# Performance work log

Measured on AMD Instinct MI355X. Metric: run time of the kernel, lower is better.

## Reference

```python
import jax, jax.numpy as jnp
import numpy as np

N_NODES, N_EDGES = 100000, 800000
F_NODE, F_EDGE, N_CLASSES = 128, 16, 10


def _lin(key, fan_in, fan_out, bias=True):
    k1, k2 = jax.random.split(key)
    W = jax.random.normal(k1, (fan_in, fan_out), jnp.float32) * 0.05
    if bias:
        b = jax.random.normal(k2, (fan_out,), jnp.float32) * 0.05
        return W, b
    return (W,)


def setup_inputs() -> dict:
    key = jax.random.key(0)
    ks = jax.random.split(key, 24)
    inp = {
        "x": jax.random.normal(ks[0], (N_NODES, F_NODE), jnp.float32),
        "edge_index": jax.random.randint(ks[1], (2, N_EDGES), 0, N_NODES, jnp.int64 if jax.config.jax_enable_x64 else jnp.int32),
        "edge_attr": jax.random.normal(ks[2], (N_EDGES, F_EDGE), jnp.float32),
    }
    dims = [(F_NODE, 128), (128, 128), (128, 256)]  # (in_channels, out_channels) per layer
    i = 3
    for li, (din, dout) in enumerate(dims, start=1):
        inp[f"Wq{li}"], inp[f"bq{li}"] = _lin(ks[i], din, dout); i += 1
        inp[f"Wk{li}"], inp[f"bk{li}"] = _lin(ks[i], din, dout); i += 1
        inp[f"Wv{li}"], inp[f"bv{li}"] = _lin(ks[i], din, dout); i += 1
        (inp[f"We{li}"],) = _lin(ks[i], F_EDGE, dout, bias=False); i += 1  # PyG lin_edge: bias=False
        inp[f"Ws{li}"], inp[f"bs{li}"] = _lin(ks[i], din, dout); i += 1  # root/skip weight
    inp["Wc"], inp["bc"] = _lin(ks[i], 256, N_CLASSES)
    return inp


def transformer_conv(x, src, dst, edge_attr, Wq, bq, Wk, bk, Wv, bv, We, Ws, bs):
    """PyG TransformerConv, heads=1, concat=True, root_weight=True."""
    N = x.shape[0]
    C = Wq.shape[1]
    q = x @ Wq + bq                      # [N, C]
    k = x @ Wk + bk                      # [N, C]
    v = x @ Wv + bv                      # [N, C]
    e = edge_attr @ We                   # [E, C] edge-conditioned term
    # per-edge attention logits: <q_i, k_j + e_ij> / sqrt(C)
    alpha = jnp.sum(q[dst] * (k[src] + e), axis=-1) / jnp.sqrt(jnp.float32(C))  # [E]
    # segment softmax over edges sharing a destination node
    m = jax.ops.segment_max(alpha, dst, num_segments=N)
    p = jnp.exp(alpha - m[dst])
    s = jax.ops.segment_sum(p, dst, num_segments=N)
    a = p / (s[dst] + 1e-16)
    # scatter-aggregate weighted messages (value_j + edge term)
    out = jax.ops.segment_sum(a[:, None] * (v[src] + e), dst, num_segments=N)  # [N, C]
    return out + x @ Ws + bs             # root/skip connection


def reference(x, edge_index, edge_attr,
              Wq1, bq1, Wk1, bk1, Wv1, bv1, We1, Ws1, bs1,
              Wq2, bq2, Wk2, bk2, Wv2, bv2, We2, Ws2, bs2,
              Wq3, bq3, Wk3, bk3, Wv3, bv3, We3, Ws3, bs3,
              Wc, bc):
    src, dst = edge_index[0], edge_index[1]
    h = transformer_conv(x, src, dst, edge_attr, Wq1, bq1, Wk1, bk1, Wv1, bv1, We1, Ws1, bs1)
    h = jax.nn.relu(h)  # dropout is identity in eval mode
    h = transformer_conv(h, src, dst, edge_attr, Wq2, bq2, Wk2, bk2, Wv2, bv2, We2, Ws2, bs2)
    h = jax.nn.relu(h)
    h = transformer_conv(h, src, dst, edge_attr, Wq3, bq3, Wk3, bk3, Wv3, bv3, We3, Ws3, bs3)
    return h @ Wc + bc                   # [N, num_classes]
```

## Files before the change

### kernel.cpp

```cpp
#include <hip/hip_runtime.h>
#include <math.h>


typedef unsigned int uint;
typedef unsigned short ushort;
typedef __bf16 bf16x8 __attribute__((ext_vector_type(8)));
typedef float f32x4 __attribute__((ext_vector_type(4)));

__device__ __forceinline__ ushort f2bf(float f) {
    uint u = __float_as_uint(f);
    u += 0x7fffu + ((u >> 16) & 1u);
    return (ushort)(u >> 16);
}
__device__ __forceinline__ float bf2f(ushort h) {
    return __uint_as_float(((uint)h) << 16);
}

__global__ void k_zero(uint* p, int n) {
    int i = blockIdx.x * 256 + threadIdx.x;
    if (i < n) p[i] = 0u;
}

__global__ void k_hist(const int* __restrict__ dst, uint* __restrict__ counts, int E, int N) {
    int e = blockIdx.x * 256 + threadIdx.x;
    if (e < E) {
        int d = dst[e];
        d = (d < 0) ? 0 : (d >= N ? N - 1 : d);
        atomicAdd(&counts[d], 1u);
    }
}

__global__ void k_scan1(const uint* __restrict__ counts, uint* __restrict__ bsum, int n) {
    __shared__ uint sm[256];
    int tid = threadIdx.x;
    int base = blockIdx.x * 1024 + tid * 4;
    uint s = 0;
#pragma unroll
    for (int j = 0; j < 4; ++j)
        if (base + j < n) s += counts[base + j];
    sm[tid] = s;
    __syncthreads();
    for (int d = 128; d > 0; d >>= 1) {
        if (tid < d) sm[tid] += sm[tid + d];
        __syncthreads();
    }
    if (tid == 0) bsum[blockIdx.x] = sm[0];
}

__global__ void k_scan2(uint* bsum, int nb) {
    if (threadIdx.x == 0 && blockIdx.x == 0) {
        uint run = 0;
        for (int i = 0; i < nb; ++i) { uint v = bsum[i]; bsum[i] = run; run += v; }
    }
}

__global__ void k_scan3(const uint* __restrict__ counts, const uint* __restrict__ bsum,
                        uint* __restrict__ row_ptr, int n, int E) {
    __shared__ uint sm[256];
    int tid = threadIdx.x;
    int base = blockIdx.x * 1024 + tid * 4;
    uint local[4];
    uint s = 0;
#pragma unroll
    for (int j = 0; j < 4; ++j) {
        local[j] = (base + j < n) ? counts[base + j] : 0u;
        s += local[j];
    }
    sm[tid] = s;
    __syncthreads();
    for (int d = 1; d < 256; d <<= 1) {
        uint v = (tid >= d) ? sm[tid - d] : 0u;
        __syncthreads();
        sm[tid] += v;
        __syncthreads();
    }
    uint run = sm[tid] - s + bsum[blockIdx.x];
#pragma unroll
    for (int j = 0; j < 4; ++j)
        if (base + j < n) { row_ptr[base + j] = run; run += local[j]; }
    if (blockIdx.x == 0 && tid == 0) row_ptr[n] = (uint)E;
}

__global__ void k_fill(const int* __restrict__ ei, const uint* __restrict__ row_ptr,
                       uint* __restrict__ cursor, int2* __restrict__ srcid, int E, int N) {
    int e = blockIdx.x * 256 + threadIdx.x;
    if (e >= E) return;
    int s = ei[e];
    int d = ei[E + e];
    s = (s < 0) ? 0 : (s >= N ? N - 1 : s);
    d = (d < 0) ? 0 : (d >= N ? N - 1 : d);
    uint idx = row_ptr[d] + atomicAdd(&cursor[d], 1u);
    srcid[idx] = make_int2(s, e);
}

__global__ void k_cvt(const float4* __restrict__ in, ushort4* __restrict__ outp, int n4) {
    int i = blockIdx.x * 256 + threadIdx.x;
    if (i >= n4) return;
    float4 v = in[i];
    ushort4 o;
    o.x = f2bf(v.x); o.y = f2bf(v.y); o.z = f2bf(v.z); o.w = f2bf(v.w);
    outp[i] = o;
}

__global__ void k_packg(const float* __restrict__ Wq, const float* __restrict__ bq,
                        const float* __restrict__ We, float* __restrict__ Wgf,
                        float* __restrict__ bgf, int C) {
    int id = blockIdx.x * 256 + threadIdx.x;
    if (id < 2048) {
        int k = id >> 4, f = id & 15;
        float s = 0.f;
        for (int c = 0; c < C; ++c) s = fmaf(Wq[k * C + c], We[f * C + c], s);
        Wgf[id] = s;
    } else if (id < 2064) {
        int f = id - 2048;
        float s = 0.f;
        for (int c = 0; c < C; ++c) s = fmaf(bq[c], We[f * C + c], s);
        bgf[f] = s;
    }
}

__global__ void k_packw(const float* __restrict__ Wq, const float* __restrict__ Wk,
                        const float* __restrict__ Wv, const float* __restrict__ Ws,
                        const float* __restrict__ Wgf, ushort* __restrict__ Bp, int C) {
    int nct = (4 * C + 16) >> 4;
    int total = 4 * nct * 512;
    int id = blockIdx.x * 256 + threadIdx.x;
    if (id >= total) return;
    int j = id & 7;
    int rest = id >> 3;
    int lane = rest & 63;
    rest >>= 6;
    int ct = rest % nct;
    int kt = rest / nct;
    int k = kt * 32 + ((lane >> 4) << 3) + j;
    int c = (ct << 4) + (lane & 15);
    float w;
    if (c < 4 * C) {
        int mat = c / C, cc = c % C;
        const float* W = (mat == 0) ? Wq : (mat == 1) ? Wk : (mat == 2) ? Wv : Ws;
        w = W[k * C + cc];
    } else {
        w = Wgf[k * 16 + (c - 4 * C)];
    }
    Bp[id] = f2bf(w);
}

__global__ void k_bias(const float* __restrict__ bq, const float* __restrict__ bk,
                       const float* __restrict__ bv, const float* __restrict__ bs,
                       const float* __restrict__ bgf, float* __restrict__ outp, int C) {
    int c = blockIdx.x * 256 + threadIdx.x;
    if (c >= 4 * C + 16) return;
    float v;
    if (c < 4 * C) {
        int mat = c / C, cc = c % C;
        const float* b = (mat == 0) ? bq : (mat == 1) ? bk : (mat == 2) ? bv : bs;
        v = b[cc];
    } else {
        v = bgf[c - 4 * C];
    }
    outp[c] = v;
}

__global__ __launch_bounds__(256) void k_gemm(const ushort* __restrict__ A,
                                              const ushort* __restrict__ Bp,
                                              const float* __restrict__ bias,
                                              ushort* __restrict__ H,
                                              ushort* __restrict__ S,
                                              ushort* __restrict__ g, int C) {
    int fourC = 4 * C, threeC = 3 * C;
    int P = fourC + 16;
    int nct = P >> 4;
    int lane = threadIdx.x & 63;
    int wave = threadIdx.x >> 6;
    int quad = lane >> 4;
    int r = lane & 15;
    int m0 = blockIdx.y << 4;
    int c0 = (blockIdx.x << 8) + (wave << 6);
    int ct0 = c0 >> 4;
    if (ct0 >= nct) return;
    int row = m0 + r;

    f32x4 acc[4];
#pragma unroll
    for (int i = 0; i < 4; ++i) acc[i] = (f32x4){0.f, 0.f, 0.f, 0.f};

#pragma unroll
    for (int kk = 0; kk < 4; ++kk) {
        bf16x8 a = *(const bf16x8*)(A + (size_t)row * 128 + kk * 32 + (quad << 3));
#pragma unroll
        for (int i = 0; i < 4; ++i) {
            if (ct0 + i < nct) {
                bf16x8 b = *(const bf16x8*)(Bp + ((size_t)((kk * nct + ct0 + i) << 6) + lane) * 8);
                acc[i] = __builtin_amdgcn_mfma_f32_16x16x32_bf16(a, b, acc[i], 0, 0, 0);
            }
        }
    }
#pragma unroll
    for (int i = 0; i < 4; ++i) {
        int cc = c0 + (i << 4) + r;
        if (cc >= P) continue;
        float bi = bias[cc];
#pragma unroll
        for (int reg = 0; reg < 4; ++reg) {
            int rr = m0 + (quad << 2) + reg;
            ushort val = f2bf(acc[i][reg] + bi);
            if (cc < threeC)      H[(size_t)rr * threeC + cc] = val;
            else if (cc < fourC)  S[(size_t)rr * C + (cc - threeC)] = val;
            else                  g[(size_t)rr * 16 + (cc - fourC)] = val;
        }
    }
}

template <int VPL>
__device__ __forceinline__ void loadbf(const ushort* p, float* o);
template <>
__device__ __forceinline__ void loadbf<2>(const ushort* p, float* o) {
    uint u = *(const uint*)p;
    o[0] = bf2f((ushort)(u & 0xffffu));
    o[1] = bf2f((ushort)(u >> 16));
}
template <>
__device__ __forceinline__ void loadbf<4>(const ushort* p, float* o) {
    uint2 u = *(const uint2*)p;
    o[0] = bf2f((ushort)(u.x & 0xffffu));
    o[1] = bf2f((ushort)(u.x >> 16));
    o[2] = bf2f((ushort)(u.y & 0xffffu));
    o[3] = bf2f((ushort)(u.y >> 16));
}

template <int C, bool RELU>
__global__ __launch_bounds__(256) void k_edge(const ushort* __restrict__ H,
                                              ushort* __restrict__ S,
                                              const ushort* __restrict__ g,
                                              const uint* __restrict__ row_ptr,
                                              const int2* __restrict__ srcid,
                                              const float* __restrict__ eattr,
                                              const float* __restrict__ We,
                                              int N, int totalWaves) {
    constexpr int VPL = C / 64;
    constexpr int THREEC = 3 * C;
    __shared__ float sWe[16 * C];
    for (int idx = threadIdx.x; idx < 16 * C; idx += 256) sWe[idx] = We[idx];
    __syncthreads();

    int lane = threadIdx.x & 63;
    int f16 = lane & 15;
    int gw = (int)((blockIdx.x * blockDim.x + threadIdx.x) >> 6);
    const float scale = (C == 128) ? 0.08838834764831843f : 0.0625f;

    for (int node = gw; node < N; node += totalWaves) {
        uint beg = row_ptr[node], end = row_ptr[node + 1];
        float q[VPL];
        loadbf<VPL>(H + (size_t)node * THREEC + lane * VPL, q);
        float gl = bf2f(g[(size_t)node * 16 + f16]);
        float m = -INFINITY, l = 0.f, w = 0.f;
        float acc[VPL];
#pragma unroll
        for (int j = 0; j < VPL; ++j) acc[j] = 0.f;

        for (uint t = beg; t < end; t += 4) {
            int rem = (int)(end - t);
            int2 se0 = srcid[t];
            int2 se1 = srcid[(rem > 1) ? t + 1 : t];
            int2 se2 = srcid[(rem > 2) ? t + 2 : t];
            int2 se3 = srcid[(rem > 3) ? t + 3 : t];
            float at0 = eattr[(size_t)se0.y * 16 + f16];
            float at1 = eattr[(size_t)se1.y * 16 + f16];
            float at2 = eattr[(size_t)se2.y * 16 + f16];
            float at3 = eattr[(size_t)se3.y * 16 + f16];
            float kv0[VPL], kv1[VPL], kv2[VPL], kv3[VPL];
            float vv0[VPL], vv1[VPL], vv2[VPL], vv3[VPL];
            loadbf<VPL>(H + (size_t)se0.x * THREEC + C + lane * VPL, kv0);
            loadbf<VPL>(H + (size_t)se1.x * THREEC + C + lane * VPL, kv1);
            loadbf<VPL>(H + (size_t)se2.x * THREEC + C + lane * VPL, kv2);
            loadbf<VPL>(H + (size_t)se3.x * THREEC + C + lane * VPL, kv3);
            loadbf<VPL>(H + (size_t)se0.x * THREEC + 2 * C + lane * VPL, vv0);
            loadbf<VPL>(H + (size_t)se1.x * THREEC + 2 * C + lane * VPL, vv1);
            loadbf<VPL>(H + (size_t)se2.x * THREEC + 2 * C + lane * VPL, vv2);
            loadbf<VPL>(H + (size_t)se3.x * THREEC + 2 * C + lane * VPL, vv3);
            float p0 = 0.25f * at0 * gl;
            float p1 = 0.25f * at1 * gl;
            float p2 = 0.25f * at2 * gl;
            float p3 = 0.25f * at3 * gl;
#pragma unroll
            for (int j = 0; j < VPL; ++j) {
                p0 = fmaf(q[j], kv0[j], p0);
                p1 = fmaf(q[j], kv1[j], p1);
                p2 = fmaf(q[j], kv2[j], p2);
                p3 = fmaf(q[j], kv3[j], p3);
            }
#pragma unroll
            for (int off = 32; off > 0; off >>= 1) {
                p0 += __shfl_xor(p0, off);
                p1 += __shfl_xor(p1, off);
                p2 += __shfl_xor(p2, off);
                p3 += __shfl_xor(p3, off);
            }
            float a0 = p0 * scale;
            float a1 = (rem > 1) ? p1 * scale : -INFINITY;
            float a2 = (rem > 2) ? p2 * scale : -INFINITY;
            float a3 = (rem > 3) ? p3 * scale : -INFINITY;
            float mn = fmaxf(m, fmaxf(fmaxf(a0, a1), fmaxf(a2, a3)));
            float sc = __expf(m - mn);
            float e0 = __expf(a0 - mn);
            float e1 = __expf(a1 - mn);
            float e2 = __expf(a2 - mn);
            float e3 = __expf(a3 - mn);
            l = l * sc + ((e0 + e1) + (e2 + e3));
#pragma unroll
            for (int j = 0; j < VPL; ++j)
                acc[j] = acc[j] * sc + ((e0 * vv0[j] + e1 * vv1[j]) + (e2 * vv2[j] + e3 * vv3[j]));
            w = w * sc + ((e0 * at0 + e1 * at1) + (e2 * at2 + e3 * at3));
            m = mn;
        }
        float inv = 1.f / (l + 1e-16f);
        float wv[16];
#pragma unroll
        for (int f = 0; f < 16; ++f) wv[f] = __shfl(w, f);
        float sk[VPL];
        loadbf<VPL>(S + (size_t)node * C + lane * VPL, sk);
#pragma unroll
        for (int j = 0; j < VPL; ++j) {
            float ew = 0.f;
#pragma unroll
            for (int f = 0; f < 16; ++f) ew = fmaf(wv[f], sWe[f * C + lane * VPL + j], ew);
            float o = (acc[j] + ew) * inv + sk[j];
            if (RELU) o = fmaxf(o, 0.f);
            S[(size_t)node * C + lane * VPL + j] = f2bf(o);
        }
    }
}

__global__ void k_cls(const ushort* __restrict__ h, const float* __restrict__ Wc,
                      const float* __restrict__ bc, float* __restrict__ outp, int N) {
    int t = blockIdx.x * 256 + threadIdx.x;
    int node = t >> 4;
    int c = t & 15;
    if (node >= N || c >= 10) return;
    const ushort* hr = h + (size_t)node * 256;
    float acc = 0.f;
#pragma unroll 4
    for (int k4 = 0; k4 < 64; ++k4) {
        uint2 u = *(const uint2*)(hr + k4 * 4);
        float h0 = bf2f((ushort)(u.x & 0xffffu));
        float h1 = bf2f((ushort)(u.x >> 16));
        float h2 = bf2f((ushort)(u.y & 0xffffu));
        float h3 = bf2f((ushort)(u.y >> 16));
        int kb = k4 * 4;
        acc = fmaf(h0, Wc[(kb + 0) * 10 + c], acc);
        acc = fmaf(h1, Wc[(kb + 1) * 10 + c], acc);
        acc = fmaf(h2, Wc[(kb + 2) * 10 + c], acc);
        acc = fmaf(h3, Wc[(kb + 3) * 10 + c], acc);
    }
    outp[node * 10 + c] = acc + bc[c];
}

extern "C" void kernel_launch(void* const* d_in, const int* in_sizes, int n_in,
                              void* d_out, int out_size, void* d_ws, size_t ws_size,
                              hipStream_t stream) {
    const float* x = (const float*)d_in[0];
    const int* ei = (const int*)d_in[1];
    const float* eattr = (const float*)d_in[2];
    const int N = in_sizes[0] / 128;
    const int E = in_sizes[1] / 2;

    const float* Wq[3], *bq[3], *Wk[3], *bk[3], *Wv[3], *bv[3], *We[3], *Ws[3], *bs[3];
    for (int li = 0; li < 3; ++li) {
        int base = 3 + li * 9;
        Wq[li] = (const float*)d_in[base + 0];
        bq[li] = (const float*)d_in[base + 1];
        Wk[li] = (const float*)d_in[base + 2];
        bk[li] = (const float*)d_in[base + 3];
        Wv[li] = (const float*)d_in[base + 4];
        bv[li] = (const float*)d_in[base + 5];
        We[li] = (const float*)d_in[base + 6];
        Ws[li] = (const float*)d_in[base + 7];
        bs[li] = (const float*)d_in[base + 8];
    }
    const float* Wc = (const float*)d_in[30];
    const float* bc = (const float*)d_in[31];

    size_t off = 0;
    char* base = (char*)d_ws;
    auto alloc = [&](size_t bytes) -> void* {
        void* p = base + off;
        off = (off + bytes + 255) & ~(size_t)255;
        return p;
    };
    ushort* SA = (ushort*)alloc((size_t)N * 256 * 2);
    ushort* SB = (ushort*)alloc((size_t)N * 128 * 2);
    ushort* H  = (ushort*)alloc((size_t)N * 768 * 2);
    ushort* gbuf = (ushort*)alloc((size_t)N * 16 * 2);
    ushort* Bp = (ushort*)alloc(140000 * 2);
    float* biasc = (float*)alloc(1040 * 4);
    float* Wgf = (float*)alloc(2048 * 4);
    float* bgf = (float*)alloc(16 * 4);
    uint* row_ptr = (uint*)alloc((size_t)(N + 1) * 4);
    uint* counts = (uint*)alloc((size_t)N * 4);
    uint* cursor = (uint*)alloc((size_t)N * 4);
    uint* bsum = (uint*)alloc(1024 * 4);
    int2* srcid = (int2*)alloc((size_t)E * 8);

    ushort* xb = SB;

    int nb = (N + 1023) / 1024;

    k_zero<<<(N + 255) / 256, 256, 0, stream>>>(counts, N);
    k_zero<<<(N + 255) / 256, 256, 0, stream>>>(cursor, N);
    k_hist<<<(E + 255) / 256, 256, 0, stream>>>(ei + E, counts, E, N);
    k_scan1<<<nb, 256, 0, stream>>>(counts, bsum, N);
    k_scan2<<<1, 64, 0, stream>>>(bsum, nb);
    k_scan3<<<nb, 256, 0, stream>>>(counts, bsum, row_ptr, N, E);
    k_fill<<<(E + 255) / 256, 256, 0, stream>>>(ei, row_ptr, cursor, srcid, E, N);

    int n4 = N * 128 / 4;
    k_cvt<<<(n4 + 255) / 256, 256, 0, stream>>>((const float4*)x, (ushort4*)xb, n4);

    const int EDGE_BLOCKS = 2048;
    const int TW = EDGE_BLOCKS * 4;

    for (int li = 0; li < 3; ++li) {
        int C = (li == 2) ? 256 : 128;
        int P = 4 * C + 16;
        int packTotal = 4 * (P >> 4) * 512;
        const ushort* A = (li == 0) ? xb : (li == 1) ? SA : SB;
        ushort* Sout = (li == 1) ? SB : SA;

        k_packg<<<9, 256, 0, stream>>>(Wq[li], bq[li], We[li], Wgf, bgf, C);
        k_packw<<<(packTotal + 255) / 256, 256, 0, stream>>>(Wq[li], Wk[li], Wv[li], Ws[li], Wgf, Bp, C);
        k_bias<<<(P + 255) / 256, 256, 0, stream>>>(bq[li], bk[li], bv[li], bs[li], bgf, biasc, C);
        k_gemm<<<dim3((P + 255) / 256, N / 16), 256, 0, stream>>>(A, Bp, biasc, H, Sout, gbuf, C);
        if (li == 2)
            k_edge<256, false><<<EDGE_BLOCKS, 256, 0, stream>>>(H, Sout, gbuf, row_ptr, srcid, eattr, We[li], N, TW);
        else
            k_edge<128, true><<<EDGE_BLOCKS, 256, 0, stream>>>(H, Sout, gbuf, row_ptr, srcid, eattr, We[li], N, TW);
    }

    k_cls<<<(N * 16 + 255) / 256, 256, 0, stream>>>(SA, Wc, bc, (float*)d_out, N);
}
```

Before: 1.149 ms.

## Split wave into four edge lanes with 16-lane rows and prefetch pipeline

Restructures the per-node edge kernel so each wave processes four edges at once, one per 16-lane quarter. Each lane now loads 16-byte vectors of K/V rows, and dot-product reductions shrink to 4 shuffle steps. The next edge's K/V is software-prefetched while the current one is computed. Per-quarter online-softmax states are merged at the end, and the We projection is read from global memory instead of shared memory. This adds more registers per lane and cross-quarter merge shuffles, which may lower occupancy.

```diff
diff --git a/kernel.cpp b/kernel.cpp
--- a/kernel.cpp
+++ b/kernel.cpp
@@ -14,6 +14,12 @@
 }
 __device__ __forceinline__ float bf2f(ushort h) {
     return __uint_as_float(((uint)h) << 16);
+}
+__device__ __forceinline__ void unpack8(uint4 t, float* o) {
+    o[0] = bf2f((ushort)(t.x & 0xffffu)); o[1] = bf2f((ushort)(t.x >> 16));
+    o[2] = bf2f((ushort)(t.y & 0xffffu)); o[3] = bf2f((ushort)(t.y >> 16));
+    o[4] = bf2f((ushort)(t.z & 0xffffu)); o[5] = bf2f((ushort)(t.z >> 16));
+    o[6] = bf2f((ushort)(t.w & 0xffffu)); o[7] = bf2f((ushort)(t.w >> 16));
 }
 
 __global__ void k_zero(uint* p, int n) {
@@ -211,23 +217,6 @@
     }
 }
 
-template <int VPL>
-__device__ __forceinline__ void loadbf(const ushort* p, float* o);
-template <>
-__device__ __forceinline__ void loadbf<2>(const ushort* p, float* o) {
-    uint u = *(const uint*)p;
-    o[0] = bf2f((ushort)(u & 0xffffu));
-    o[1] = bf2f((ushort)(u >> 16));
-}
-template <>
-__device__ __forceinline__ void loadbf<4>(const ushort* p, float* o) {
-    uint2 u = *(const uint2*)p;
-    o[0] = bf2f((ushort)(u.x & 0xffffu));
-    o[1] = bf2f((ushort)(u.x >> 16));
-    o[2] = bf2f((ushort)(u.y & 0xffffu));
-    o[3] = bf2f((ushort)(u.y >> 16));
-}
-
 template <int C, bool RELU>
 __global__ __launch_bounds__(256) void k_edge(const ushort* __restrict__ H,
                                               ushort* __restrict__ S,
@@ -237,96 +226,136 @@
                                               const float* __restrict__ eattr,
                                               const float* __restrict__ We,
                                               int N, int totalWaves) {
-    constexpr int VPL = C / 64;
-    constexpr int THREEC = 3 * C;
-    __shared__ float sWe[16 * C];
-    for (int idx = threadIdx.x; idx < 16 * C; idx += 256) sWe[idx] = We[idx];
-    __syncthreads();
-
+    constexpr int VR = C / 16;
+    constexpr int NU4 = VR / 8;
+    constexpr int TH = 3 * C;
+    const float scale = (C == 128) ? 0.08838834764831843f : 0.0625f;
     int lane = threadIdx.x & 63;
-    int f16 = lane & 15;
+    int sub = lane & 15;
+    int quad = lane >> 4;
     int gw = (int)((blockIdx.x * blockDim.x + threadIdx.x) >> 6);
-    const float scale = (C == 128) ? 0.08838834764831843f : 0.0625f;
 
     for (int node = gw; node < N; node += totalWaves) {
         uint beg = row_ptr[node], end = row_ptr[node + 1];
-        float q[VPL];
-        loadbf<VPL>(H + (size_t)node * THREEC + lane * VPL, q);
-        float gl = bf2f(g[(size_t)node * 16 + f16]);
-        float m = -INFINITY, l = 0.f, w = 0.f;
-        float acc[VPL];
-#pragma unroll
-        for (int j = 0; j < VPL; ++j) acc[j] = 0.f;
-
-        for (uint t = beg; t < end; t += 4) {
-            int rem = (int)(end - t);
-            int2 se0 = srcid[t];
-            int2 se1 = srcid[(rem > 1) ? t + 1 : t];
-            int2 se2 = srcid[(rem > 2) ? t + 2 : t];
-            int2 se3 = srcid[(rem > 3) ? t + 3 : t];
-            float at0 = eattr[(size_t)se0.y * 16 + f16];
-            float at1 = eattr[(size_t)se1.y * 16 + f16];
-            float at2 = eattr[(size_t)se2.y * 16 + f16];
-            float at3 = eattr[(size_t)se3.y * 16 + f16];
-            float kv0[VPL], kv1[VPL], kv2[VPL], kv3[VPL];
-            float vv0[VPL], vv1[VPL], vv2[VPL], vv3[VPL];
-            loadbf<VPL>(H + (size_t)se0.x * THREEC + C + lane * VPL, kv0);
-            loadbf<VPL>(H + (size_t)se1.x * THREEC + C + lane * VPL, kv1);
-            loadbf<VPL>(H + (size_t)se2.x * THREEC + C + lane * VPL, kv2);
-            loadbf<VPL>(H + (size_t)se3.x * THREEC + C + lane * VPL, kv3);
-            loadbf<VPL>(H + (size_t)se0.x * THREEC + 2 * C + lane * VPL, vv0);
-            loadbf<VPL>(H + (size_t)se1.x * THREEC + 2 * C + lane * VPL, vv1);
-            loadbf<VPL>(H + (size_t)se2.x * THREEC + 2 * C + lane * VPL, vv2);
-            loadbf<VPL>(H + (size_t)se3.x * THREEC + 2 * C + lane * VPL, vv3);
-            float p0 = 0.25f * at0 * gl;
-            float p1 = 0.25f * at1 * gl;
-            float p2 = 0.25f * at2 * gl;
-            float p3 = 0.25f * at3 * gl;
-#pragma unroll
-            for (int j = 0; j < VPL; ++j) {
-                p0 = fmaf(q[j], kv0[j], p0);
-                p1 = fmaf(q[j], kv1[j], p1);
-                p2 = fmaf(q[j], kv2[j], p2);
-                p3 = fmaf(q[j], kv3[j], p3);
-            }
-#pragma unroll
-            for (int off = 32; off > 0; off >>= 1) {
-                p0 += __shfl_xor(p0, off);
-                p1 += __shfl_xor(p1, off);
-                p2 += __shfl_xor(p2, off);
-                p3 += __shfl_xor(p3, off);
-            }
-            float a0 = p0 * scale;
-            float a1 = (rem > 1) ? p1 * scale : -INFINITY;
-            float a2 = (rem > 2) ? p2 * scale : -INFINITY;
-            float a3 = (rem > 3) ? p3 * scale : -INFINITY;
-            float mn = fmaxf(m, fmaxf(fmaxf(a0, a1), fmaxf(a2, a3)));
-            float sc = __expf(m - mn);
-            float e0 = __expf(a0 - mn);
-            float e1 = __expf(a1 - mn);
-            float e2 = __expf(a2 - mn);
-            float e3 = __expf(a3 - mn);
-            l = l * sc + ((e0 + e1) + (e2 + e3));
-#pragma unroll
-            for (int j = 0; j < VPL; ++j)
-                acc[j] = acc[j] * sc + ((e0 * vv0[j] + e1 * vv1[j]) + (e2 * vv2[j] + e3 * vv3[j]));
-            w = w * sc + ((e0 * at0 + e1 * at1) + (e2 * at2 + e3 * at3));
-            m = mn;
+        float q[VR];
+        {
+            const uint4* qp = (const uint4*)(H + (size_t)node * TH + sub * VR);
+#pragma unroll
+            for (int u = 0; u < NU4; ++u) { uint4 tt = qp[u]; unpack8(tt, q + u * 8); }
+        }
+        float gl = bf2f(g[(size_t)node * 16 + sub]);
+        float m = -1e30f, l = 0.f, w = 0.f;
+        float acc[VR];
+#pragma unroll
+        for (int j = 0; j < VR; ++j) acc[j] = 0.f;
+
+        if (beg < end) {
+            uint last = end - 1;
+            uint i1 = beg + quad;     if (i1 > last) i1 = last;
+            uint i2 = beg + 4 + quad; if (i2 > last) i2 = last;
+            int2 seA = srcid[i1];
+            int2 seB = srcid[i2];
+            float atA = eattr[(size_t)seA.y * 16 + sub];
+            uint4 kA[NU4], vA[NU4];
+            {
+                const uint4* kp = (const uint4*)(H + (size_t)seA.x * TH + C + sub * VR);
+                const uint4* vp = (const uint4*)(H + (size_t)seA.x * TH + 2 * C + sub * VR);
+#pragma unroll
+                for (int u = 0; u < NU4; ++u) { kA[u] = kp[u]; vA[u] = vp[u]; }
+            }
+            for (uint t = beg; t < end; t += 4) {
+                uint i3 = t + 8 + (uint)quad; if (i3 > last) i3 = last;
+                int2 seC = srcid[i3];
+                float atB = eattr[(size_t)seB.y * 16 + sub];
+                uint4 kB[NU4], vB[NU4];
+                {
+                    const uint4* kp = (const uint4*)(H + (size_t)seB.x * TH + C + sub * VR);
+                    const uint4* vp = (const uint4*)(H + (size_t)seB.x * TH + 2 * C + sub * VR);
+#pragma unroll
+                    for (int u = 0; u < NU4; ++u) { kB[u] = kp[u]; vB[u] = vp[u]; }
+                }
+                bool valid = (t + (uint)quad) < end;
+                float kf[VR];
+#pragma unroll
+                for (int u = 0; u < NU4; ++u) unpack8(kA[u], kf + u * 8);
+                float p = atA * gl;
+#pragma unroll
+                for (int j = 0; j < VR; ++j) p = fmaf(q[j], kf[j], p);
+                p += __shfl_xor(p, 1);
+                p += __shfl_xor(p, 2);
+                p += __shfl_xor(p, 4);
+                p += __shfl_xor(p, 8);
+                float alpha = valid ? p * scale : -1e30f;
+                float mn = fmaxf(m, alpha);
+                float sc = __expf(m - mn);
+                float e = valid ? __expf(alpha - mn) : 0.f;
+                l = l * sc + e;
+                w = fmaf(e, atA, w * sc);
+                float vf[VR];
+#pragma unroll
+                for (int u = 0; u < NU4; ++u) unpack8(vA[u], vf + u * 8);
+#pragma unroll
+                for (int j = 0; j < VR; ++j) acc[j] = fmaf(e, vf[j], acc[j] * sc);
+                m = mn;
+                seB = seC;
+                atA = atB;
+#pragma unroll
+                for (int u = 0; u < NU4; ++u) { kA[u] = kB[u]; vA[u] = vB[u]; }
+            }
+            float mm = fmaxf(m, __shfl_xor(m, 16));
+            mm = fmaxf(mm, __shfl_xor(mm, 32));
+            float r = __expf(m - mm);
+            l *= r; l += __shfl_xor(l, 16); l += __shfl_xor(l, 32);
+            w *= r; w += __shfl_xor(w, 16); w += __shfl_xor(w, 32);
+#pragma unroll
+            for (int j = 0; j < VR; ++j) {
+                float a = acc[j] * r;
+                a += __shfl_xor(a, 16);
+                a += __shfl_xor(a, 32);
+                acc[j] = a;
+            }
         }
         float inv = 1.f / (l + 1e-16f);
-        float wv[16];
-#pragma unroll
-        for (int f = 0; f < 16; ++f) wv[f] = __shfl(w, f);
-        float sk[VPL];
-        loadbf<VPL>(S + (size_t)node * C + lane * VPL, sk);
-#pragma unroll
-        for (int j = 0; j < VPL; ++j) {
-            float ew = 0.f;
-#pragma unroll
-            for (int f = 0; f < 16; ++f) ew = fmaf(wv[f], sWe[f * C + lane * VPL + j], ew);
-            float o = (acc[j] + ew) * inv + sk[j];
-            if (RELU) o = fmaxf(o, 0.f);
-            S[(size_t)node * C + lane * VPL + j] = f2bf(o);
+        float ew[VR];
+#pragma unroll
+        for (int j = 0; j < VR; ++j) ew[j] = 0.f;
+#pragma unroll
+        for (int i = 0; i < 4; ++i) {
+            int f = quad * 4 + i;
+            float wf = __shfl(w, f);
+            const float* wrow = We + f * C + sub * VR;
+#pragma unroll
+            for (int u = 0; u < VR / 4; ++u) {
+                float4 cv = *(const float4*)(wrow + u * 4);
+                ew[u * 4 + 0] = fmaf(wf, cv.x, ew[u * 4 + 0]);
+                ew[u * 4 + 1] = fmaf(wf, cv.y, ew[u * 4 + 1]);
+                ew[u * 4 + 2] = fmaf(wf, cv.z, ew[u * 4 + 2]);
+                ew[u * 4 + 3] = fmaf(wf, cv.w, ew[u * 4 + 3]);
+            }
+        }
+#pragma unroll
+        for (int j = 0; j < VR; ++j) {
+            ew[j] += __shfl_xor(ew[j], 16);
+            ew[j] += __shfl_xor(ew[j], 32);
+        }
+        if (quad == 0) {
+            ushort* srow = S + (size_t)node * C + sub * VR;
+#pragma unroll
+            for (int u = 0; u < NU4; ++u) {
+                uint4 skv = *(const uint4*)(srow + u * 8);
+                float sk[8];
+                unpack8(skv, sk);
+                uint4 ov;
+                uint* op = (uint*)&ov;
+#pragma unroll
+                for (int h = 0; h < 4; ++h) {
+                    float o0 = (acc[u * 8 + 2 * h] + ew[u * 8 + 2 * h]) * inv + sk[2 * h];
+                    float o1 = (acc[u * 8 + 2 * h + 1] + ew[u * 8 + 2 * h + 1]) * inv + sk[2 * h + 1];
+                    if (RELU) { o0 = fmaxf(o0, 0.f); o1 = fmaxf(o1, 0.f); }
+                    op[h] = (uint)f2bf(o0) | ((uint)f2bf(o1) << 16);
+                }
+                *(uint4*)(srow + u * 8) = ov;
+            }
         }
     }
 }
```

After: 1.126 ms. 2.0% less time.
